# Kernel optimization log

Measured on AMD Instinct MI355X. Metric: run time of the kernel, lower is better.

## Reference

```python
import jax, jax.numpy as jnp
import numpy as np

QMAX_W = 127.0   # symmetric int8 for weights
QMAX_A = 255.0   # asymmetric uint8 for activations


def setup_inputs() -> dict:
    key = jax.random.key(0)
    k1, k2, k3 = jax.random.split(key, 3)
    B, S, K, N = 4, 2048, 4096, 4096
    x = jax.random.normal(k1, (B, S, K), dtype=jnp.float32)
    weight = jax.random.normal(k2, (N, K), dtype=jnp.float32) * (1.0 / np.sqrt(K))
    bias = jax.random.normal(k3, (N,), dtype=jnp.float32) * 0.02
    return {"x": x, "weight": weight, "bias": bias}


def reference(x, weight, bias):
    N, K = weight.shape
    # --- weight quantization: row-wise symmetric int8 (absmax / 127) ---
    row_absmax = jnp.max(jnp.abs(weight), axis=1)            # [N]
    row_scales = jnp.where(row_absmax > 0, row_absmax / QMAX_W, 1.0)
    Wq = jnp.clip(jnp.round(weight / row_scales[:, None]), -QMAX_W, QMAX_W)  # int8 values, kept f32 for GEMM

    # --- activation quantization: per-token (column of X^T) asymmetric uint8 ---
    orig_shape = x.shape
    X = x.reshape(-1, K)                                     # [M, K]
    xmin = jnp.min(X, axis=1)                                # [M]
    xmax = jnp.max(X, axis=1)
    rng = xmax - xmin
    col_scales = jnp.where(rng > 0, rng / QMAX_A, 1.0)       # [M]
    col_zps = jnp.round(-xmin / col_scales)                  # [M]
    Xq = jnp.clip(jnp.round(X / col_scales[:, None]) + col_zps[:, None], 0.0, QMAX_A)  # uint8 values

    # --- int GEMM with zero-point correction + dequant: Y[m,n] = s_a[m]*s_w[n]*sum_k (Xq-zp)[m,k]*Wq[n,k] ---
    acc = jnp.einsum('mk,nk->mn', Xq - col_zps[:, None], Wq)  # [M, N]
    Y = acc * (col_scales[:, None] * row_scales[None, :]) + bias
    return Y.reshape(orig_shape[:-1] + (N,))
```

## Files before the change

kernel.cpp:

```cpp
#include <hip/hip_runtime.h>
#include <stdint.h>
#include <stddef.h>

typedef __attribute__((ext_vector_type(4))) int i32x4;

#define BM 128
#define BN 128
#define BK 64

__device__ __forceinline__ void gload_lds16(const void* g, void* l) {
    __builtin_amdgcn_global_load_lds(
        (const __attribute__((address_space(1))) void*)g,
        (__attribute__((address_space(3))) void*)l,
        16, 0, 0);
}

__device__ __forceinline__ float waveMaxF(float v) {
#pragma unroll
    for (int o = 32; o > 0; o >>= 1) v = fmaxf(v, __shfl_down(v, o, 64));
    return v;
}
__device__ __forceinline__ float waveMinF(float v) {
#pragma unroll
    for (int o = 32; o > 0; o >>= 1) v = fminf(v, __shfl_down(v, o, 64));
    return v;
}
__device__ __forceinline__ int waveSumI(int v) {
#pragma unroll
    for (int o = 32; o > 0; o >>= 1) v += __shfl_down(v, o, 64);
    return v;
}

__global__ void __launch_bounds__(256) wquant_kernel(
    const float* __restrict__ W, int8_t* __restrict__ Wq,
    float* __restrict__ rscale, int* __restrict__ rsum, int K) {
    const int n = blockIdx.x;
    const float4* row = (const float4*)(W + (size_t)n * K);
    const int K4 = K >> 2;

    float amax = 0.f;
    for (int i = threadIdx.x; i < K4; i += 256) {
        float4 f = row[i];
        amax = fmaxf(amax, fmaxf(fmaxf(fabsf(f.x), fabsf(f.y)),
                                 fmaxf(fabsf(f.z), fabsf(f.w))));
    }
    __shared__ float smax[4];
    __shared__ int ssum[4];
    amax = waveMaxF(amax);
    const int wave = threadIdx.x >> 6;
    const int lane = threadIdx.x & 63;
    if (lane == 0) smax[wave] = amax;
    __syncthreads();
    amax = fmaxf(fmaxf(smax[0], smax[1]), fmaxf(smax[2], smax[3]));
    const float scale = (amax > 0.f) ? (amax / 127.0f) : 1.0f;

    int lsum = 0;
    char4* out = (char4*)(Wq + (size_t)n * K);
    for (int i = threadIdx.x; i < K4; i += 256) {
        float4 f = row[i];
        float q0 = fminf(fmaxf(rintf(f.x / scale), -127.f), 127.f);
        float q1 = fminf(fmaxf(rintf(f.y / scale), -127.f), 127.f);
        float q2 = fminf(fmaxf(rintf(f.z / scale), -127.f), 127.f);
        float q3 = fminf(fmaxf(rintf(f.w / scale), -127.f), 127.f);
        int i0 = (int)q0, i1 = (int)q1, i2 = (int)q2, i3 = (int)q3;
        lsum += i0 + i1 + i2 + i3;
        char4 c;
        c.x = (signed char)i0; c.y = (signed char)i1;
        c.z = (signed char)i2; c.w = (signed char)i3;
        out[i] = c;
    }
    lsum = waveSumI(lsum);
    if (lane == 0) ssum[wave] = lsum;
    __syncthreads();
    if (threadIdx.x == 0) {
        rsum[n] = ssum[0] + ssum[1] + ssum[2] + ssum[3];
        rscale[n] = scale;
    }
}

__global__ void __launch_bounds__(256) aquant_kernel(
    const float* __restrict__ X, int8_t* __restrict__ Xq,
    float* __restrict__ cscale, int* __restrict__ azp, int K) {
    const int m = blockIdx.x;
    const float4* row = (const float4*)(X + (size_t)m * K);
    const int K4 = K >> 2;

    float vmin = 3.402823466e38f, vmax = -3.402823466e38f;
    for (int i = threadIdx.x; i < K4; i += 256) {
        float4 f = row[i];
        vmin = fminf(vmin, fminf(fminf(f.x, f.y), fminf(f.z, f.w)));
        vmax = fmaxf(vmax, fmaxf(fmaxf(f.x, f.y), fmaxf(f.z, f.w)));
    }
    __shared__ float smin[4], smax[4];
    vmin = waveMinF(vmin);
    vmax = waveMaxF(vmax);
    const int wave = threadIdx.x >> 6;
    const int lane = threadIdx.x & 63;
    if (lane == 0) { smin[wave] = vmin; smax[wave] = vmax; }
    __syncthreads();
    vmin = fminf(fminf(smin[0], smin[1]), fminf(smin[2], smin[3]));
    vmax = fmaxf(fmaxf(smax[0], smax[1]), fmaxf(smax[2], smax[3]));

    const float rng = vmax - vmin;
    const float scale = (rng > 0.f) ? (rng / 255.0f) : 1.0f;
    const float zp = rintf(-vmin / scale);

    char4* out = (char4*)(Xq + (size_t)m * K);
    for (int i = threadIdx.x; i < K4; i += 256) {
        float4 f = row[i];
        float q0 = fminf(fmaxf(rintf(f.x / scale) + zp, 0.f), 255.f);
        float q1 = fminf(fmaxf(rintf(f.y / scale) + zp, 0.f), 255.f);
        float q2 = fminf(fmaxf(rintf(f.z / scale) + zp, 0.f), 255.f);
        float q3 = fminf(fmaxf(rintf(f.w / scale) + zp, 0.f), 255.f);
        char4 c;
        c.x = (signed char)((int)q0 - 128);
        c.y = (signed char)((int)q1 - 128);
        c.z = (signed char)((int)q2 - 128);
        c.w = (signed char)((int)q3 - 128);
        out[i] = c;
    }
    if (threadIdx.x == 0) {
        cscale[m] = scale;
        azp[m] = 128 - (int)zp;
    }
}

__global__ void __launch_bounds__(256) gemm_i8_kernel(
    const int8_t* __restrict__ A, const int8_t* __restrict__ B,
    float* __restrict__ Y,
    const float* __restrict__ cs, const int* __restrict__ azp,
    const float* __restrict__ rs, const int* __restrict__ rsum,
    const float* __restrict__ bias, int M, int N, int K) {
    __shared__ int8_t As[BM * BK];
    __shared__ int8_t Bs[BN * BK];

    const int tid = threadIdx.x;
    const int lane = tid & 63;
    const int wave = tid >> 6;
    const int wm = wave & 1;
    const int wn = wave >> 1;
    const int quad = lane >> 4;
    const int lr = lane & 15;

    const int bm = blockIdx.x * BM;
    const int bn = blockIdx.y * BN;

    const int8_t* Ag = A + (size_t)bm * K;
    const int8_t* Bg = B + (size_t)bn * K;

    const int srow = tid >> 2;
    const int scol = (tid & 3) << 4;

    i32x4 acc[4][4] = {};

    for (int k0 = 0; k0 < K; k0 += BK) {
        gload_lds16(Ag + (size_t)srow * K + (k0 + scol), &As[srow * BK + scol]);
        gload_lds16(Ag + (size_t)(srow + 64) * K + (k0 + scol), &As[(srow + 64) * BK + scol]);
        gload_lds16(Bg + (size_t)srow * K + (k0 + scol), &Bs[srow * BK + scol]);
        gload_lds16(Bg + (size_t)(srow + 64) * K + (k0 + scol), &Bs[(srow + 64) * BK + scol]);
        __syncthreads();

        i32x4 af[4], bf[4];
#pragma unroll
        for (int i = 0; i < 4; ++i)
            af[i] = *(const i32x4*)&As[(wm * 64 + i * 16 + lr) * BK + quad * 16];
#pragma unroll
        for (int j = 0; j < 4; ++j)
            bf[j] = *(const i32x4*)&Bs[(wn * 64 + j * 16 + lr) * BK + quad * 16];

#pragma unroll
        for (int i = 0; i < 4; ++i)
#pragma unroll
            for (int j = 0; j < 4; ++j)
                acc[i][j] = __builtin_amdgcn_mfma_i32_16x16x64_i8(af[i], bf[j], acc[i][j], 0, 0, 0);

        __syncthreads();
    }

#pragma unroll
    for (int i = 0; i < 4; ++i) {
        const int mb = bm + wm * 64 + i * 16 + quad * 4;
#pragma unroll
        for (int r = 0; r < 4; ++r) {
            const int m = mb + r;
            const float csm = cs[m];
            const int az = azp[m];
            float* yrow = Y + (size_t)m * N;
#pragma unroll
            for (int j = 0; j < 4; ++j) {
                const int n = bn + wn * 64 + j * 16 + lr;
                const int tot = acc[i][j][r] + az * rsum[n];
                yrow[n] = fmaf((float)tot, csm * rs[n], bias[n]);
            }
        }
    }
}

extern "C" void kernel_launch(void* const* d_in, const int* in_sizes, int n_in,
                              void* d_out, int out_size, void* d_ws, size_t ws_size,
                              hipStream_t stream) {
    const float* x = (const float*)d_in[0];
    const float* w = (const float*)d_in[1];
    const float* bias = (const float*)d_in[2];
    float* y = (float*)d_out;

    const int N = in_sizes[2];
    const int K = in_sizes[1] / N;
    const int M = in_sizes[0] / K;

    uint8_t* ws = (uint8_t*)d_ws;
    int8_t* Wq = (int8_t*)ws;
    int8_t* Xq = (int8_t*)(ws + (size_t)N * K);
    uint8_t* p = ws + (size_t)N * K + (size_t)M * K;
    p = (uint8_t*)(((uintptr_t)p + 255) & ~(uintptr_t)255);
    float* rscale = (float*)p;  p += (size_t)N * sizeof(float);
    int*   rsum   = (int*)p;    p += (size_t)N * sizeof(int);
    float* cscale = (float*)p;  p += (size_t)M * sizeof(float);
    int*   azp    = (int*)p;    p += (size_t)M * sizeof(int);

    wquant_kernel<<<N, 256, 0, stream>>>(w, Wq, rscale, rsum, K);
    aquant_kernel<<<M, 256, 0, stream>>>(x, Xq, cscale, azp, K);

    dim3 grid(M / BM, N / BN);
    gemm_i8_kernel<<<grid, 256, 0, stream>>>(Xq, Wq, y, cscale, azp,
                                             rscale, rsum, bias, M, N, K);
}
```

Before: 500.7 us.

## Merge quant kernels into one wave-per-row launch and use 32x32 int8 MFMA with swizzled LDS

Both quantization kernels are merged into a single launch in which each wave handles one row. This drops a kernel launch and the block-level shared-memory reductions, and divides by the scale are replaced with a multiply by its reciprocal. The GEMM switches from 16x16x64 to 32x32x32 int8 MFMA with an XOR-swizzled LDS layout to cut bank conflicts, and the epilogue hoists the per-column scale, row-sum and bias loads. The reciprocal multiply may differ from exact division by one rounding step in rare cases.

```diff
diff --git a/kernel.cpp b/kernel.cpp
--- a/kernel.cpp
+++ b/kernel.cpp
@@ -3,6 +3,7 @@
 #include <stddef.h>
 
 typedef __attribute__((ext_vector_type(4))) int i32x4;
+typedef __attribute__((ext_vector_type(16))) int i32x16;
 
 #define BM 128
 #define BN 128
@@ -17,111 +18,92 @@
 
 __device__ __forceinline__ float waveMaxF(float v) {
 #pragma unroll
-    for (int o = 32; o > 0; o >>= 1) v = fmaxf(v, __shfl_down(v, o, 64));
+    for (int o = 32; o > 0; o >>= 1) v = fmaxf(v, __shfl_xor(v, o, 64));
     return v;
 }
 __device__ __forceinline__ float waveMinF(float v) {
 #pragma unroll
-    for (int o = 32; o > 0; o >>= 1) v = fminf(v, __shfl_down(v, o, 64));
+    for (int o = 32; o > 0; o >>= 1) v = fminf(v, __shfl_xor(v, o, 64));
     return v;
 }
 __device__ __forceinline__ int waveSumI(int v) {
 #pragma unroll
-    for (int o = 32; o > 0; o >>= 1) v += __shfl_down(v, o, 64);
+    for (int o = 32; o > 0; o >>= 1) v += __shfl_xor(v, o, 64);
     return v;
 }
 
-__global__ void __launch_bounds__(256) wquant_kernel(
-    const float* __restrict__ W, int8_t* __restrict__ Wq,
-    float* __restrict__ rscale, int* __restrict__ rsum, int K) {
-    const int n = blockIdx.x;
-    const float4* row = (const float4*)(W + (size_t)n * K);
-    const int K4 = K >> 2;
-
-    float amax = 0.f;
-    for (int i = threadIdx.x; i < K4; i += 256) {
-        float4 f = row[i];
-        amax = fmaxf(amax, fmaxf(fmaxf(fabsf(f.x), fabsf(f.y)),
-                                 fmaxf(fabsf(f.z), fabsf(f.w))));
-    }
-    __shared__ float smax[4];
-    __shared__ int ssum[4];
-    amax = waveMaxF(amax);
+__global__ void __launch_bounds__(256) quant_kernel(
+    const float* __restrict__ W, const float* __restrict__ X,
+    int8_t* __restrict__ Wq, int8_t* __restrict__ Xq,
+    float* __restrict__ rscale, int* __restrict__ rsum,
+    float* __restrict__ cscale, int* __restrict__ azp,
+    int K, int N, int M, int NBW) {
     const int wave = threadIdx.x >> 6;
     const int lane = threadIdx.x & 63;
-    if (lane == 0) smax[wave] = amax;
-    __syncthreads();
-    amax = fmaxf(fmaxf(smax[0], smax[1]), fmaxf(smax[2], smax[3]));
-    const float scale = (amax > 0.f) ? (amax / 127.0f) : 1.0f;
-
-    int lsum = 0;
-    char4* out = (char4*)(Wq + (size_t)n * K);
-    for (int i = threadIdx.x; i < K4; i += 256) {
-        float4 f = row[i];
-        float q0 = fminf(fmaxf(rintf(f.x / scale), -127.f), 127.f);
-        float q1 = fminf(fmaxf(rintf(f.y / scale), -127.f), 127.f);
-        float q2 = fminf(fmaxf(rintf(f.z / scale), -127.f), 127.f);
-        float q3 = fminf(fmaxf(rintf(f.w / scale), -127.f), 127.f);
-        int i0 = (int)q0, i1 = (int)q1, i2 = (int)q2, i3 = (int)q3;
-        lsum += i0 + i1 + i2 + i3;
-        char4 c;
-        c.x = (signed char)i0; c.y = (signed char)i1;
-        c.z = (signed char)i2; c.w = (signed char)i3;
-        out[i] = c;
-    }
-    lsum = waveSumI(lsum);
-    if (lane == 0) ssum[wave] = lsum;
-    __syncthreads();
-    if (threadIdx.x == 0) {
-        rsum[n] = ssum[0] + ssum[1] + ssum[2] + ssum[3];
-        rscale[n] = scale;
-    }
-}
-
-__global__ void __launch_bounds__(256) aquant_kernel(
-    const float* __restrict__ X, int8_t* __restrict__ Xq,
-    float* __restrict__ cscale, int* __restrict__ azp, int K) {
-    const int m = blockIdx.x;
-    const float4* row = (const float4*)(X + (size_t)m * K);
     const int K4 = K >> 2;
 
-    float vmin = 3.402823466e38f, vmax = -3.402823466e38f;
-    for (int i = threadIdx.x; i < K4; i += 256) {
-        float4 f = row[i];
-        vmin = fminf(vmin, fminf(fminf(f.x, f.y), fminf(f.z, f.w)));
-        vmax = fmaxf(vmax, fmaxf(fmaxf(f.x, f.y), fmaxf(f.z, f.w)));
-    }
-    __shared__ float smin[4], smax[4];
-    vmin = waveMinF(vmin);
-    vmax = waveMaxF(vmax);
-    const int wave = threadIdx.x >> 6;
-    const int lane = threadIdx.x & 63;
-    if (lane == 0) { smin[wave] = vmin; smax[wave] = vmax; }
-    __syncthreads();
-    vmin = fminf(fminf(smin[0], smin[1]), fminf(smin[2], smin[3]));
-    vmax = fmaxf(fmaxf(smax[0], smax[1]), fmaxf(smax[2], smax[3]));
-
-    const float rng = vmax - vmin;
-    const float scale = (rng > 0.f) ? (rng / 255.0f) : 1.0f;
-    const float zp = rintf(-vmin / scale);
-
-    char4* out = (char4*)(Xq + (size_t)m * K);
-    for (int i = threadIdx.x; i < K4; i += 256) {
-        float4 f = row[i];
-        float q0 = fminf(fmaxf(rintf(f.x / scale) + zp, 0.f), 255.f);
-        float q1 = fminf(fmaxf(rintf(f.y / scale) + zp, 0.f), 255.f);
-        float q2 = fminf(fmaxf(rintf(f.z / scale) + zp, 0.f), 255.f);
-        float q3 = fminf(fmaxf(rintf(f.w / scale) + zp, 0.f), 255.f);
-        char4 c;
-        c.x = (signed char)((int)q0 - 128);
-        c.y = (signed char)((int)q1 - 128);
-        c.z = (signed char)((int)q2 - 128);
-        c.w = (signed char)((int)q3 - 128);
-        out[i] = c;
-    }
-    if (threadIdx.x == 0) {
-        cscale[m] = scale;
-        azp[m] = 128 - (int)zp;
+    if ((int)blockIdx.x < NBW) {
+        const int n = blockIdx.x * 4 + wave;
+        if (n >= N) return;
+        const float4* src = (const float4*)(W + (size_t)n * K);
+
+        float amax = 0.f;
+        for (int i = lane; i < K4; i += 64) {
+            float4 f = src[i];
+            amax = fmaxf(amax, fmaxf(fmaxf(fabsf(f.x), fabsf(f.y)),
+                                     fmaxf(fabsf(f.z), fabsf(f.w))));
+        }
+        amax = waveMaxF(amax);
+        const float scale = (amax > 0.f) ? (amax / 127.0f) : 1.0f;
+        const float inv = 1.0f / scale;
+
+        int lsum = 0;
+        char4* out = (char4*)(Wq + (size_t)n * K);
+        for (int i = lane; i < K4; i += 64) {
+            float4 f = src[i];
+            int i0 = (int)fminf(fmaxf(rintf(f.x * inv), -127.f), 127.f);
+            int i1 = (int)fminf(fmaxf(rintf(f.y * inv), -127.f), 127.f);
+            int i2 = (int)fminf(fmaxf(rintf(f.z * inv), -127.f), 127.f);
+            int i3 = (int)fminf(fmaxf(rintf(f.w * inv), -127.f), 127.f);
+            lsum += i0 + i1 + i2 + i3;
+            char4 c;
+            c.x = (signed char)i0; c.y = (signed char)i1;
+            c.z = (signed char)i2; c.w = (signed char)i3;
+            out[i] = c;
+        }
+        lsum = waveSumI(lsum);
+        if (lane == 0) { rsum[n] = lsum; rscale[n] = scale; }
+    } else {
+        const int m = ((int)blockIdx.x - NBW) * 4 + wave;
+        if (m >= M) return;
+        const float4* src = (const float4*)(X + (size_t)m * K);
+
+        float vmin = 3.402823466e38f, vmax = -3.402823466e38f;
+        for (int i = lane; i < K4; i += 64) {
+            float4 f = src[i];
+            vmin = fminf(vmin, fminf(fminf(f.x, f.y), fminf(f.z, f.w)));
+            vmax = fmaxf(vmax, fmaxf(fmaxf(f.x, f.y), fmaxf(f.z, f.w)));
+        }
+        vmin = waveMinF(vmin);
+        vmax = waveMaxF(vmax);
+        const float rng = vmax - vmin;
+        const float scale = (rng > 0.f) ? (rng / 255.0f) : 1.0f;
+        const float zp = rintf(-vmin / scale);
+        const float inv = 1.0f / scale;
+
+        char4* out = (char4*)(Xq + (size_t)m * K);
+        for (int i = lane; i < K4; i += 64) {
+            float4 f = src[i];
+            int q0 = (int)fminf(fmaxf(rintf(f.x * inv) + zp, 0.f), 255.f) - 128;
+            int q1 = (int)fminf(fmaxf(rintf(f.y * inv) + zp, 0.f), 255.f) - 128;
+            int q2 = (int)fminf(fmaxf(rintf(f.z * inv) + zp, 0.f), 255.f) - 128;
+            int q3 = (int)fminf(fmaxf(rintf(f.w * inv) + zp, 0.f), 255.f) - 128;
+            char4 c;
+            c.x = (signed char)q0; c.y = (signed char)q1;
+            c.z = (signed char)q2; c.w = (signed char)q3;
+            out[i] = c;
+        }
+        if (lane == 0) { cscale[m] = scale; azp[m] = 128 - (int)zp; }
     }
 }
 
@@ -139,8 +121,8 @@
     const int wave = tid >> 6;
     const int wm = wave & 1;
     const int wn = wave >> 1;
-    const int quad = lane >> 4;
-    const int lr = lane & 15;
+    const int ml = lane & 31;
+    const int kh = lane >> 5;
 
     const int bm = blockIdx.x * BM;
     const int bn = blockIdx.y * BN;
@@ -149,51 +131,72 @@
     const int8_t* Bg = B + (size_t)bn * K;
 
     const int srow = tid >> 2;
-    const int scol = (tid & 3) << 4;
-
-    i32x4 acc[4][4] = {};
+    const int pcol = tid & 3;
+    const int sgoff = ((pcol ^ (srow & 3)) << 4);
+    const int sloff = srow * BK + (pcol << 4);
+
+    int aoff[2][2], boff[2][2];
+#pragma unroll
+    for (int i = 0; i < 2; ++i)
+#pragma unroll
+        for (int ks = 0; ks < 2; ++ks) {
+            const int Ra = wm * 64 + i * 32 + ml;
+            aoff[i][ks] = Ra * BK + (((ks * 2 + kh) ^ (Ra & 3)) << 4);
+            const int Rb = wn * 64 + i * 32 + ml;
+            boff[i][ks] = Rb * BK + (((ks * 2 + kh) ^ (Rb & 3)) << 4);
+        }
+
+    i32x16 acc[2][2] = {};
 
     for (int k0 = 0; k0 < K; k0 += BK) {
-        gload_lds16(Ag + (size_t)srow * K + (k0 + scol), &As[srow * BK + scol]);
-        gload_lds16(Ag + (size_t)(srow + 64) * K + (k0 + scol), &As[(srow + 64) * BK + scol]);
-        gload_lds16(Bg + (size_t)srow * K + (k0 + scol), &Bs[srow * BK + scol]);
-        gload_lds16(Bg + (size_t)(srow + 64) * K + (k0 + scol), &Bs[(srow + 64) * BK + scol]);
+        gload_lds16(Ag + (size_t)srow * K + (k0 + sgoff), &As[sloff]);
+        gload_lds16(Ag + (size_t)(srow + 64) * K + (k0 + sgoff), &As[64 * BK + sloff]);
+        gload_lds16(Bg + (size_t)srow * K + (k0 + sgoff), &Bs[sloff]);
+        gload_lds16(Bg + (size_t)(srow + 64) * K + (k0 + sgoff), &Bs[64 * BK + sloff]);
         __syncthreads();
 
-        i32x4 af[4], bf[4];
-#pragma unroll
-        for (int i = 0; i < 4; ++i)
-            af[i] = *(const i32x4*)&As[(wm * 64 + i * 16 + lr) * BK + quad * 16];
-#pragma unroll
-        for (int j = 0; j < 4; ++j)
-            bf[j] = *(const i32x4*)&Bs[(wn * 64 + j * 16 + lr) * BK + quad * 16];
-
-#pragma unroll
-        for (int i = 0; i < 4; ++i)
-#pragma unroll
-            for (int j = 0; j < 4; ++j)
-                acc[i][j] = __builtin_amdgcn_mfma_i32_16x16x64_i8(af[i], bf[j], acc[i][j], 0, 0, 0);
+        i32x4 af[2][2], bf[2][2];
+#pragma unroll
+        for (int i = 0; i < 2; ++i)
+#pragma unroll
+            for (int ks = 0; ks < 2; ++ks) {
+                af[i][ks] = *(const i32x4*)&As[aoff[i][ks]];
+                bf[i][ks] = *(const i32x4*)&Bs[boff[i][ks]];
+            }
+
+#pragma unroll
+        for (int ks = 0; ks < 2; ++ks)
+#pragma unroll
+            for (int i = 0; i < 2; ++i)
+#pragma unroll
+                for (int j = 0; j < 2; ++j)
+                    acc[i][j] = __builtin_amdgcn_mfma_i32_32x32x32_i8(
+                        af[i][ks], bf[j][ks], acc[i][j], 0, 0, 0);
 
         __syncthreads();
     }
 
-#pragma unroll
-    for (int i = 0; i < 4; ++i) {
-        const int mb = bm + wm * 64 + i * 16 + quad * 4;
-#pragma unroll
-        for (int r = 0; r < 4; ++r) {
-            const int m = mb + r;
+    int nidx[2], rsumn[2];
+    float rsn[2], bsn[2];
+#pragma unroll
+    for (int j = 0; j < 2; ++j) {
+        const int n = bn + wn * 64 + j * 32 + ml;
+        nidx[j] = n; rsn[j] = rs[n]; rsumn[j] = rsum[n]; bsn[j] = bias[n];
+    }
+#pragma unroll
+    for (int i = 0; i < 2; ++i)
+#pragma unroll
+        for (int r = 0; r < 16; ++r) {
+            const int m = bm + wm * 64 + i * 32 + (r & 3) + 8 * (r >> 2) + 4 * kh;
             const float csm = cs[m];
             const int az = azp[m];
             float* yrow = Y + (size_t)m * N;
 #pragma unroll
-            for (int j = 0; j < 4; ++j) {
-                const int n = bn + wn * 64 + j * 16 + lr;
-                const int tot = acc[i][j][r] + az * rsum[n];
-                yrow[n] = fmaf((float)tot, csm * rs[n], bias[n]);
+            for (int j = 0; j < 2; ++j) {
+                const int tot = acc[i][j][r] + az * rsumn[j];
+                yrow[nidx[j]] = fmaf((float)tot, csm * rsn[j], bsn[j]);
             }
         }
-    }
 }
 
 extern "C" void kernel_launch(void* const* d_in, const int* in_sizes, int n_in,
@@ -218,8 +221,10 @@
     float* cscale = (float*)p;  p += (size_t)M * sizeof(float);
     int*   azp    = (int*)p;    p += (size_t)M * sizeof(int);
 
-    wquant_kernel<<<N, 256, 0, stream>>>(w, Wq, rscale, rsum, K);
-    aquant_kernel<<<M, 256, 0, stream>>>(x, Xq, cscale, azp, K);
+    const int NBW = (N + 3) / 4;
+    const int NBA = (M + 3) / 4;
+    quant_kernel<<<NBW + NBA, 256, 0, stream>>>(w, x, Wq, Xq, rscale, rsum,
+                                                cscale, azp, K, N, M, NBW);
 
     dim3 grid(M / BM, N / BN);
     gemm_i8_kernel<<<grid, 256, 0, stream>>>(Xq, Wq, y, cscale, azp,
```

Result: no change. 502.5 us (+0.3%).
